# Performance work log

Hardware: AMD Instinct MI355X
Metric: run time of the kernel (lower is better)

Reference implementation:

```python
import jax, jax.numpy as jnp
import numpy as np

EPS = 1e-06


def _phi(x):
    # elu_feature_map: elu(x) + 1  (strictly positive features)
    return jax.nn.elu(x) + 1.0


def setup_inputs() -> dict:
    key = jax.random.key(0)
    k1, k2, k3 = jax.random.split(key, 3)
    N, L, H, D = 4, 4096, 12, 64
    q = jax.random.normal(k1, (N, L, H, D), dtype=jnp.float32)
    k = jax.random.normal(k2, (N, L, H, D), dtype=jnp.float32)
    v = jax.random.normal(k3, (N, L, H, D), dtype=jnp.float32)
    return {"q": q, "k": k, "v": v}


def _causal_linear_attention(q, k, v):
    qf = _phi(q)  # [N,L,H,D]
    kf = _phi(k)
    # normalizer: z_l = q_l . (sum_{s<=l} k_s) + eps
    z = jnp.einsum('nlhd,nlhd->nlh', qf, jnp.cumsum(kf, axis=1)) + EPS
    # causal_dot_product: sequential cumulative outer-product scan over L
    q_l = jnp.moveaxis(qf, 1, 0)  # [L,N,H,D]
    k_l = jnp.moveaxis(kf, 1, 0)
    v_l = jnp.moveaxis(v, 1, 0)   # [L,N,H,M]
    N, H, D = qf.shape[0], qf.shape[2], qf.shape[3]
    M = v.shape[3]
    S0 = jnp.zeros((N, H, D, M), dtype=qf.dtype)

    def step(S, qkv):
        ql, kl, vl = qkv
        S = S + jnp.einsum('nhd,nhm->nhdm', kl, vl)  # accumulate k v^T
        o = jnp.einsum('nhd,nhdm->nhm', ql, S)       # q . S
        return S, o

    _, out = jax.lax.scan(step, S0, (q_l, k_l, v_l))  # out: [L,N,H,M]
    out = jnp.moveaxis(out, 0, 1)  # [N,L,H,M]
    return out / z[..., None]


def reference(q, k, v):
    # mask=None path of LinearAttention.forward (causal linear attention)
    return _causal_linear_attention(q, k, v)
```

## Files before the change

### kernel.cpp

```cpp
#include <hip/hip_runtime.h>


#define NBATCH 4
#define LSEQ   4096
#define NHEAD  12
#define DDIM   64
#define LSTRIDE (NHEAD * DDIM)
#define NH     (NBATCH * NHEAD)
#define EPSF   1e-6f
#define CHUNK  64
#define NUMC   (LSEQ / CHUNK)
#define PPART  32
#define CPP    (NUMC / PPART)
#define SB     72

typedef __attribute__((ext_vector_type(8))) short bf16x8;
typedef __attribute__((ext_vector_type(4))) float f32x4;

__device__ __forceinline__ float phi(float x) { return x > 0.f ? x + 1.f : __expf(x); }
__device__ __forceinline__ float4 phi4(float4 x) {
    float4 r = {phi(x.x), phi(x.y), phi(x.z), phi(x.w)};
    return r;
}

__device__ __forceinline__ unsigned short f2bf(float x) {
    union { float f; unsigned u; } v; v.f = x;
    unsigned r = v.u + 0x7fffu + ((v.u >> 16) & 1u);
    return (unsigned short)(r >> 16);
}
__device__ __forceinline__ float bf2f(short s) {
    union { float f; unsigned u; } v; v.u = ((unsigned)(unsigned short)s) << 16;
    return v.f;
}
__device__ __forceinline__ uint2 pack4(float4 a) {
    uint2 r;
    r.x = (unsigned)f2bf(a.x) | ((unsigned)f2bf(a.y) << 16);
    r.y = (unsigned)f2bf(a.z) | ((unsigned)f2bf(a.w) << 16);
    return r;
}
__device__ __forceinline__ bf16x8 packbf8(float4 a, float4 b) {
    union { bf16x8 v; uint2 u[2]; } r;
    r.u[0] = pack4(a);
    r.u[1] = pack4(b);
    return r.v;
}

__device__ __forceinline__ float4 xpose4(float4 x, int lane) {
    const bool b0 = (lane >> 4) & 1, b1 = (lane >> 5) & 1;
    float s0 = b0 ? x.x : x.y;
    float s1 = b0 ? x.z : x.w;
    s0 = __shfl_xor(s0, 16);
    s1 = __shfl_xor(s1, 16);
    float4 y;
    if (b0) { y.x = s0;  y.y = x.y; y.z = s1;  y.w = x.w; }
    else    { y.x = x.x; y.y = s0;  y.z = x.z; y.w = s1;  }
    float t0 = b1 ? y.x : y.z;
    float t1 = b1 ? y.y : y.w;
    t0 = __shfl_xor(t0, 32);
    t1 = __shfl_xor(t1, 32);
    float4 z;
    if (b1) { z.x = t0;  z.y = t1;  z.z = y.z; z.w = y.w; }
    else    { z.x = y.x; z.y = y.y; z.z = t0;  z.w = t1;  }
    return z;
}

__device__ __forceinline__ void swapbit(uint2& A, uint2& B, int m, bool hi) {
    uint2 t;
    t.x = hi ? A.x : B.x;
    t.y = hi ? A.y : B.y;
    t.x = (unsigned)__shfl_xor((int)t.x, m);
    t.y = (unsigned)__shfl_xor((int)t.y, m);
    if (hi) { A.x = t.x; A.y = t.y; } else { B.x = t.x; B.y = t.y; }
}

__global__ __launch_bounds__(256) void k_pass1(const float* __restrict__ qin,
                                               const float* __restrict__ kin,
                                               const float* __restrict__ vin,
                                               float* __restrict__ kvws,
                                               float* __restrict__ ksws,
                                               float* __restrict__ zws,
                                               float* __restrict__ out) {
    __shared__ short sK [64 * SB];
    __shared__ short sKT[64 * SB];
    __shared__ short sVT[64 * SB];
    __shared__ short sST[64 * SB];
    __shared__ float sKs[64];

    const int b = blockIdx.x, seq = b / PPART, p = b % PPART;
    const int n0 = seq / NHEAD, h0 = seq % NHEAD;
    const int t = threadIdx.x;
    const int lane = t & 63, w = t >> 6;
    const int nn = lane & 15, qq = lane >> 4;
    const int c4 = nn << 2;
    const bool b4 = (lane >> 4) & 1, b5 = (lane >> 5) & 1;

    float4 kreg[4], vreg[4];
    auto LOADKV = [&](int cc) {
        const int gb = ((n0 * LSEQ + (p * CPP + cc) * CHUNK) * NHEAD + h0) * DDIM;
#pragma unroll
        for (int rep = 0; rep < 4; ++rep) {
            const int r16 = rep * 16 + 4 * w + qq;
            kreg[rep] = *(const float4*)(kin + gb + r16 * LSTRIDE + c4);
            vreg[rep] = *(const float4*)(vin + gb + r16 * LSTRIDE + c4);
        }
    };
    auto LOADQ = [&](int cc, bf16x8& o0, bf16x8& o1) {
        const float* qp = qin + ((n0 * LSEQ + (p * CPP + cc) * CHUNK) * NHEAD + h0) * DDIM
                        + (16 * w + nn) * LSTRIDE;
        float4 a = phi4(*(const float4*)(qp + qq * 8));
        float4 bq = phi4(*(const float4*)(qp + qq * 8 + 4));
        float4 cq = phi4(*(const float4*)(qp + 32 + qq * 8));
        float4 dq = phi4(*(const float4*)(qp + 32 + qq * 8 + 4));
        o0 = packbf8(a, bq);
        o1 = packbf8(cq, dq);
    };

    bf16x8 qf0, qf1, qfn0, qfn1;
    LOADKV(0);
    LOADQ(0, qf0, qf1);
    if (t < 64) sKs[t] = 0.f;

    f32x4 Sreg[4] = {{0,0,0,0},{0,0,0,0},{0,0,0,0},{0,0,0,0}};
    float ksTot = 0.f;
    const int iRow = 16 * w + nn;

    for (int cc = 0; cc < CPP; ++cc) {
        const int gbase = ((n0 * LSEQ + (p * CPP + cc) * CHUNK) * NHEAD + h0) * DDIM;
#pragma unroll
        for (int rep = 0; rep < 4; ++rep) {
            const int row = rep * 16 + 4 * w + qq;
            const int l0 = rep * 16 + 4 * w;
            float4 kp = phi4(kreg[rep]);
            *(uint2*)(sK + row * SB + c4) = pack4(kp);
            float4 kt = xpose4(kp, lane);
            *(uint2*)(sKT + (c4 + qq) * SB + l0) = pack4(kt);
            float4 vt = xpose4(vreg[rep], lane);
            *(uint2*)(sVT + (c4 + qq) * SB + l0) = pack4(vt);
        }
        __syncthreads();

        if (cc + 1 < CPP) {
            LOADKV(cc + 1);
            LOADQ(cc + 1, qfn0, qfn1);
        }

        uint2 W[4];
        float zpart = 0.f;
#pragma unroll
        for (int ct = 0; ct < 4; ++ct) {
            bf16x8 kf0 = *(const bf16x8*)(sK + (16 * ct + nn) * SB + qq * 8);
            bf16x8 kf1 = *(const bf16x8*)(sK + (16 * ct + nn) * SB + 32 + qq * 8);
            f32x4 acc = {0.f, 0.f, 0.f, 0.f};
            acc = __builtin_amdgcn_mfma_f32_16x16x32_bf16(kf0, qf0, acc, 0, 0, 0);
            acc = __builtin_amdgcn_mfma_f32_16x16x32_bf16(kf1, qf1, acc, 0, 0, 0);
            float4 mv;
            mv.x = (16 * ct + 4 * qq + 0 <= iRow) ? acc[0] : 0.f;
            mv.y = (16 * ct + 4 * qq + 1 <= iRow) ? acc[1] : 0.f;
            mv.z = (16 * ct + 4 * qq + 2 <= iRow) ? acc[2] : 0.f;
            mv.w = (16 * ct + 4 * qq + 3 <= iRow) ? acc[3] : 0.f;
            zpart += mv.x + mv.y + mv.z + mv.w;
            W[ct] = pack4(mv);
        }
        zpart += __shfl_xor(zpart, 16);
        zpart += __shfl_xor(zpart, 32);
        float zi = zpart;
        if (cc) {
            float zq = 0.f;
#pragma unroll
            for (int j = 0; j < 8; ++j) {
                zq += bf2f(qf0[j]) * sKs[qq * 8 + j];
                zq += bf2f(qf1[j]) * sKs[32 + qq * 8 + j];
            }
            zq += __shfl_xor(zq, 16);
            zq += __shfl_xor(zq, 32);
            zi += zq;
        }

        swapbit(W[0], W[1], 32, b5);
        swapbit(W[2], W[3], 32, b5);
        swapbit(W[0], W[1], 16, b4);
        swapbit(W[2], W[3], 16, b4);
        union U8 { unsigned u[4]; bf16x8 v; };
        U8 a0, a1;
        a0.u[0] = W[0].x; a0.u[1] = W[0].y; a0.u[2] = W[1].x; a0.u[3] = W[1].y;
        a1.u[0] = W[2].x; a1.u[1] = W[2].y; a1.u[2] = W[3].x; a1.u[3] = W[3].y;
        const bf16x8 amB0 = a0.v;
        const bf16x8 amB1 = a1.v;

        f32x4 o[4] = {{0,0,0,0},{0,0,0,0},{0,0,0,0},{0,0,0,0}};
        bf16x8 av0 = *(const bf16x8*)(sVT + iRow * SB + qq * 8);
        bf16x8 av1 = *(const bf16x8*)(sVT + iRow * SB + 32 + qq * 8);
        float ksc = 0.f;
#pragma unroll
        for (int ct = 0; ct < 4; ++ct) {
            bf16x8 vf0 = *(const bf16x8*)(sVT + (16 * ct + nn) * SB + qq * 8);
            bf16x8 vf1 = *(const bf16x8*)(sVT + (16 * ct + nn) * SB + 32 + qq * 8);
            o[ct] = __builtin_amdgcn_mfma_f32_16x16x32_bf16(vf0, amB0, o[ct], 0, 0, 0);
            o[ct] = __builtin_amdgcn_mfma_f32_16x16x32_bf16(vf1, amB1, o[ct], 0, 0, 0);
            if (cc) {
                bf16x8 sf0 = *(const bf16x8*)(sST + (16 * ct + nn) * SB + qq * 8);
                bf16x8 sf1 = *(const bf16x8*)(sST + (16 * ct + nn) * SB + 32 + qq * 8);
                o[ct] = __builtin_amdgcn_mfma_f32_16x16x32_bf16(sf0, qf0, o[ct], 0, 0, 0);
                o[ct] = __builtin_amdgcn_mfma_f32_16x16x32_bf16(sf1, qf1, o[ct], 0, 0, 0);
            }
            bf16x8 kt0 = *(const bf16x8*)(sKT + (16 * ct + nn) * SB + qq * 8);
            bf16x8 kt1 = *(const bf16x8*)(sKT + (16 * ct + nn) * SB + 32 + qq * 8);
            Sreg[ct] = __builtin_amdgcn_mfma_f32_16x16x32_bf16(av0, kt0, Sreg[ct], 0, 0, 0);
            Sreg[ct] = __builtin_amdgcn_mfma_f32_16x16x32_bf16(av1, kt1, Sreg[ct], 0, 0, 0);
            if (ct == w) {
                float s = 0.f;
#pragma unroll
                for (int j = 0; j < 8; ++j) s += bf2f(kt0[j]) + bf2f(kt1[j]);
                s += __shfl_xor(s, 16);
                s += __shfl_xor(s, 32);
                ksc = s;
            }
        }
        ksTot += ksc;

        float* orow = out + gbase + iRow * LSTRIDE;
#pragma unroll
        for (int ct = 0; ct < 4; ++ct)
            *(f32x4*)(orow + 16 * ct + 4 * qq) = o[ct];
        if (qq == 0)
            zws[seq * LSEQ + (p * CPP + cc) * CHUNK + iRow] = zi;

        __syncthreads();
        if (cc + 1 < CPP) {
#pragma unroll
            for (int ct = 0; ct < 4; ++ct)
#pragma unroll
                for (int r = 0; r < 4; ++r)
                    sST[(16 * w + 4 * qq + r) * SB + 16 * ct + nn] = (short)f2bf(Sreg[ct][r]);
            if (qq == 0) sKs[16 * w + nn] += ksc;
            qf0 = qfn0;
            qf1 = qfn1;
        }
    }

    float* kvb = kvws + (size_t)b * (DDIM * DDIM);
#pragma unroll
    for (int ct = 0; ct < 4; ++ct)
#pragma unroll
        for (int r = 0; r < 4; ++r)
            kvb[(16 * w + 4 * qq + r) * DDIM + 16 * ct + nn] = Sreg[ct][r];
    if (qq == 0) ksws[b * DDIM + 16 * w + nn] = ksTot;
}

__global__ __launch_bounds__(64) void k_scanP(float* __restrict__ kv,
                                              float* __restrict__ ksum) {
    const int bid = blockIdx.x;
    const int seq = bid >> 4, part16 = bid & 15;
    const int t = threadIdx.x;
    float4* base = (float4*)(kv + (size_t)seq * PPART * DDIM * DDIM) + part16 * 64 + t;
    float4 S = {0.f, 0.f, 0.f, 0.f};
    for (int b0 = 0; b0 < PPART; b0 += 8) {
        float4 x[8];
#pragma unroll
        for (int j = 0; j < 8; ++j) x[j] = base[(b0 + j) * (DDIM * DDIM / 4)];
#pragma unroll
        for (int j = 0; j < 8; ++j) {
            base[(b0 + j) * (DDIM * DDIM / 4)] = S;
            S.x += x[j].x; S.y += x[j].y; S.z += x[j].z; S.w += x[j].w;
        }
    }
    if (part16 == 0) {
        float* kb = ksum + (size_t)seq * PPART * DDIM + t;
        float s = 0.f;
        for (int b0 = 0; b0 < PPART; b0 += 8) {
            float xs[8];
#pragma unroll
            for (int j = 0; j < 8; ++j) xs[j] = kb[(b0 + j) * DDIM];
#pragma unroll
            for (int j = 0; j < 8; ++j) { kb[(b0 + j) * DDIM] = s; s += xs[j]; }
        }
    }
}

__global__ __launch_bounds__(256) void k_fix(const float* __restrict__ qin,
                                             const float* __restrict__ kvws,
                                             const float* __restrict__ ksws,
                                             const float* __restrict__ zws,
                                             float* __restrict__ out) {
    __shared__ short sST[64 * SB];
    __shared__ float sKs[64];

    const int cg = blockIdx.x;
    const int seq = cg / NUMC, c = cg % NUMC, p = c / CPP;
    const int n0 = seq / NHEAD, h0 = seq % NHEAD;
    const int t = threadIdx.x;
    const int lane = t & 63, w = t >> 6;
    const int nn = lane & 15, qq = lane >> 4;
    const int c4 = nn << 2;
    const int gbase = ((n0 * LSEQ + c * CHUNK) * NHEAD + h0) * DDIM;
    const int iRow = 16 * w + nn;

    if (t < 64) sKs[t] = ksws[(seq * PPART + p) * DDIM + t];

    const float* Sg = kvws + (size_t)(seq * PPART + p) * (DDIM * DDIM);
#pragma unroll
    for (int rep = 0; rep < 4; ++rep) {
        const int row = rep * 16 + 4 * w + qq;
        float4 sv = *(const float4*)(Sg + row * DDIM + c4);
        *(uint2*)(sST + row * SB + c4) = pack4(sv);
    }

    const float* qp = qin + gbase + iRow * LSTRIDE;
    float4 a  = phi4(*(const float4*)(qp + qq * 8));
    float4 bq = phi4(*(const float4*)(qp + qq * 8 + 4));
    float4 cq = phi4(*(const float4*)(qp + 32 + qq * 8));
    float4 dq = phi4(*(const float4*)(qp + 32 + qq * 8 + 4));
    bf16x8 qf0 = packbf8(a, bq);
    bf16x8 qf1 = packbf8(cq, dq);

    float* orow = out + gbase + iRow * LSTRIDE;
    f32x4 o[4];
#pragma unroll
    for (int ct = 0; ct < 4; ++ct)
        o[ct] = *(const f32x4*)(orow + 16 * ct + 4 * qq);
    const float zl = zws[seq * LSEQ + c * CHUNK + iRow];
    __syncthreads();

    float zq = 0.f;
#pragma unroll
    for (int j = 0; j < 8; ++j) {
        zq += bf2f(qf0[j]) * sKs[qq * 8 + j];
        zq += bf2f(qf1[j]) * sKs[32 + qq * 8 + j];
    }
    zq += __shfl_xor(zq, 16);
    zq += __shfl_xor(zq, 32);

#pragma unroll
    for (int ct = 0; ct < 4; ++ct) {
        bf16x8 sf0 = *(const bf16x8*)(sST + (16 * ct + nn) * SB + qq * 8);
        bf16x8 sf1 = *(const bf16x8*)(sST + (16 * ct + nn) * SB + 32 + qq * 8);
        o[ct] = __builtin_amdgcn_mfma_f32_16x16x32_bf16(sf0, qf0, o[ct], 0, 0, 0);
        o[ct] = __builtin_amdgcn_mfma_f32_16x16x32_bf16(sf1, qf1, o[ct], 0, 0, 0);
    }

    const float invz = 1.f / (zl + zq + EPSF);
#pragma unroll
    for (int ct = 0; ct < 4; ++ct) {
        f32x4 r = o[ct];
        r[0] *= invz; r[1] *= invz; r[2] *= invz; r[3] *= invz;
        *(f32x4*)(orow + 16 * ct + 4 * qq) = r;
    }
}

__global__ __launch_bounds__(64) void k_seq(const float* __restrict__ qin,
                                            const float* __restrict__ kin,
                                            const float* __restrict__ vin,
                                            float* __restrict__ out) {
    const int seq = blockIdx.x;
    const int n = seq / NHEAD, h = seq % NHEAD;
    const int lane = threadIdx.x;
    float Scol[DDIM];
#pragma unroll
    for (int d = 0; d < DDIM; ++d) Scol[d] = 0.0f;
    float kc = 0.0f;
    __shared__ float qk[2 * DDIM];
    int base = (n * LSEQ * NHEAD + h) * DDIM + lane;
    for (int i = 0; i < LSEQ; ++i) {
        float qval = phi(qin[base]);
        float kval = phi(kin[base]);
        float vval = vin[base];
        kc += kval;
        float zp = qval * kc;
#pragma unroll
        for (int off = 32; off > 0; off >>= 1) zp += __shfl_xor(zp, off, 64);
        float z = zp + EPSF;
        qk[2 * lane] = kval;
        qk[2 * lane + 1] = qval;
        __syncthreads();
        const float4* qk4 = (const float4*)qk;
        float acc = 0.0f;
#pragma unroll
        for (int d2 = 0; d2 < DDIM / 2; ++d2) {
            float4 t0 = qk4[d2];
            int d = 2 * d2;
            Scol[d]     += t0.x * vval;  acc += t0.y * Scol[d];
            Scol[d + 1] += t0.z * vval;  acc += t0.w * Scol[d + 1];
        }
        out[base] = acc / z;
        base += LSTRIDE;
        __syncthreads();
    }
}

extern "C" void kernel_launch(void* const* d_in, const int* in_sizes, int n_in,
                              void* d_out, int out_size, void* d_ws, size_t ws_size,
                              hipStream_t stream) {
    const float* q = (const float*)d_in[0];
    const float* k = (const float*)d_in[1];
    const float* v = (const float*)d_in[2];
    float* out = (float*)d_out;
    float* ws  = (float*)d_ws;

    const size_t need = ((size_t)NH * PPART * (DDIM * DDIM + DDIM)
                        + (size_t)NH * LSEQ) * sizeof(float);
    if (ws_size >= need) {
        float* kv   = ws;
        float* ksum = kv + (size_t)NH * PPART * DDIM * DDIM;
        float* zws  = ksum + (size_t)NH * PPART * DDIM;
        k_pass1<<<NH * PPART, 256, 0, stream>>>(q, k, v, kv, ksum, zws, out);
        k_scanP<<<NH * 16,     64, 0, stream>>>(kv, ksum);
        k_fix  <<<NH * NUMC,  256, 0, stream>>>(q, kv, ksum, zws, out);
    } else {
        k_seq<<<NH, 64, 0, stream>>>(q, k, v, out);
    }
}
```

Baseline: 224.5 us.

## Make chunk pass fully parallel with one block per chunk

The first pass previously processed two chunks per block sequentially, carrying the running KV state and key sums between chunks. Each block now handles a single 64-row chunk, writes a per-chunk KV state and key sum, and leaves all cross-chunk work to the scan and fix kernels. This doubles the block count and drops the in-block serial dependency. In exchange the KV workspace doubles, the scan kernel now walks 64 chunk states instead of 32, and the fix kernel does the inter-chunk correction for every chunk, including those the first pass used to handle.

```diff
diff --git a/kernel.cpp b/kernel.cpp
--- a/kernel.cpp
+++ b/kernel.cpp
@@ -10,8 +10,6 @@
 #define EPSF   1e-6f
 #define CHUNK  64
 #define NUMC   (LSEQ / CHUNK)
-#define PPART  32
-#define CPP    (NUMC / PPART)
 #define SB     72
 
 typedef __attribute__((ext_vector_type(8))) short bf16x8;
@@ -73,7 +71,7 @@
     if (hi) { A.x = t.x; A.y = t.y; } else { B.x = t.x; B.y = t.y; }
 }
 
-__global__ __launch_bounds__(256) void k_pass1(const float* __restrict__ qin,
+__global__ __launch_bounds__(256) void k_chunk(const float* __restrict__ qin,
                                                const float* __restrict__ kin,
                                                const float* __restrict__ vin,
                                                float* __restrict__ kvws,
@@ -83,160 +81,108 @@
     __shared__ short sK [64 * SB];
     __shared__ short sKT[64 * SB];
     __shared__ short sVT[64 * SB];
-    __shared__ short sST[64 * SB];
-    __shared__ float sKs[64];
-
-    const int b = blockIdx.x, seq = b / PPART, p = b % PPART;
+
+    const int b = blockIdx.x, seq = b / NUMC, c = b % NUMC;
     const int n0 = seq / NHEAD, h0 = seq % NHEAD;
     const int t = threadIdx.x;
     const int lane = t & 63, w = t >> 6;
     const int nn = lane & 15, qq = lane >> 4;
     const int c4 = nn << 2;
     const bool b4 = (lane >> 4) & 1, b5 = (lane >> 5) & 1;
+    const int gbase = ((n0 * LSEQ + c * CHUNK) * NHEAD + h0) * DDIM;
+    const int iRow = 16 * w + nn;
 
     float4 kreg[4], vreg[4];
-    auto LOADKV = [&](int cc) {
-        const int gb = ((n0 * LSEQ + (p * CPP + cc) * CHUNK) * NHEAD + h0) * DDIM;
-#pragma unroll
-        for (int rep = 0; rep < 4; ++rep) {
-            const int r16 = rep * 16 + 4 * w + qq;
-            kreg[rep] = *(const float4*)(kin + gb + r16 * LSTRIDE + c4);
-            vreg[rep] = *(const float4*)(vin + gb + r16 * LSTRIDE + c4);
+#pragma unroll
+    for (int rep = 0; rep < 4; ++rep) {
+        const int r16 = rep * 16 + 4 * w + qq;
+        kreg[rep] = *(const float4*)(kin + gbase + r16 * LSTRIDE + c4);
+        vreg[rep] = *(const float4*)(vin + gbase + r16 * LSTRIDE + c4);
+    }
+    const float* qp = qin + gbase + iRow * LSTRIDE;
+    float4 qa = *(const float4*)(qp + qq * 8);
+    float4 qb = *(const float4*)(qp + qq * 8 + 4);
+    float4 qc = *(const float4*)(qp + 32 + qq * 8);
+    float4 qd = *(const float4*)(qp + 32 + qq * 8 + 4);
+    const bf16x8 qf0 = packbf8(phi4(qa), phi4(qb));
+    const bf16x8 qf1 = packbf8(phi4(qc), phi4(qd));
+
+#pragma unroll
+    for (int rep = 0; rep < 4; ++rep) {
+        const int row = rep * 16 + 4 * w + qq;
+        const int l0 = rep * 16 + 4 * w;
+        float4 kp = phi4(kreg[rep]);
+        *(uint2*)(sK + row * SB + c4) = pack4(kp);
+        float4 kt = xpose4(kp, lane);
+        *(uint2*)(sKT + (c4 + qq) * SB + l0) = pack4(kt);
+        float4 vt = xpose4(vreg[rep], lane);
+        *(uint2*)(sVT + (c4 + qq) * SB + l0) = pack4(vt);
+    }
+    __syncthreads();
+
+    uint2 W[4];
+    float zpart = 0.f;
+#pragma unroll
+    for (int ct = 0; ct < 4; ++ct) {
+        bf16x8 kf0 = *(const bf16x8*)(sK + (16 * ct + nn) * SB + qq * 8);
+        bf16x8 kf1 = *(const bf16x8*)(sK + (16 * ct + nn) * SB + 32 + qq * 8);
+        f32x4 acc = {0.f, 0.f, 0.f, 0.f};
+        acc = __builtin_amdgcn_mfma_f32_16x16x32_bf16(kf0, qf0, acc, 0, 0, 0);
+        acc = __builtin_amdgcn_mfma_f32_16x16x32_bf16(kf1, qf1, acc, 0, 0, 0);
+        float4 mv;
+        mv.x = (16 * ct + 4 * qq + 0 <= iRow) ? acc[0] : 0.f;
+        mv.y = (16 * ct + 4 * qq + 1 <= iRow) ? acc[1] : 0.f;
+        mv.z = (16 * ct + 4 * qq + 2 <= iRow) ? acc[2] : 0.f;
+        mv.w = (16 * ct + 4 * qq + 3 <= iRow) ? acc[3] : 0.f;
+        zpart += mv.x + mv.y + mv.z + mv.w;
+        W[ct] = pack4(mv);
+    }
+    zpart += __shfl_xor(zpart, 16);
+    zpart += __shfl_xor(zpart, 32);
+    const float zi = zpart;
+
+    swapbit(W[0], W[1], 32, b5);
+    swapbit(W[2], W[3], 32, b5);
+    swapbit(W[0], W[1], 16, b4);
+    swapbit(W[2], W[3], 16, b4);
+    union U8 { unsigned u[4]; bf16x8 v; };
+    U8 a0, a1;
+    a0.u[0] = W[0].x; a0.u[1] = W[0].y; a0.u[2] = W[1].x; a0.u[3] = W[1].y;
+    a1.u[0] = W[2].x; a1.u[1] = W[2].y; a1.u[2] = W[3].x; a1.u[3] = W[3].y;
+    const bf16x8 amB0 = a0.v;
+    const bf16x8 amB1 = a1.v;
+
+    f32x4 o[4]    = {{0,0,0,0},{0,0,0,0},{0,0,0,0},{0,0,0,0}};
+    f32x4 Sreg[4] = {{0,0,0,0},{0,0,0,0},{0,0,0,0},{0,0,0,0}};
+    bf16x8 av0 = *(const bf16x8*)(sVT + iRow * SB + qq * 8);
+    bf16x8 av1 = *(const bf16x8*)(sVT + iRow * SB + 32 + qq * 8);
+    float ksc = 0.f;
+#pragma unroll
+    for (int ct = 0; ct < 4; ++ct) {
+        bf16x8 vf0 = *(const bf16x8*)(sVT + (16 * ct + nn) * SB + qq * 8);
+        bf16x8 vf1 = *(const bf16x8*)(sVT + (16 * ct + nn) * SB + 32 + qq * 8);
+        o[ct] = __builtin_amdgcn_mfma_f32_16x16x32_bf16(vf0, amB0, o[ct], 0, 0, 0);
+        o[ct] = __builtin_amdgcn_mfma_f32_16x16x32_bf16(vf1, amB1, o[ct], 0, 0, 0);
+        bf16x8 kt0 = *(const bf16x8*)(sKT + (16 * ct + nn) * SB + qq * 8);
+        bf16x8 kt1 = *(const bf16x8*)(sKT + (16 * ct + nn) * SB + 32 + qq * 8);
+        Sreg[ct] = __builtin_amdgcn_mfma_f32_16x16x32_bf16(av0, kt0, Sreg[ct], 0, 0, 0);
+        Sreg[ct] = __builtin_amdgcn_mfma_f32_16x16x32_bf16(av1, kt1, Sreg[ct], 0, 0, 0);
+        if (ct == w) {
+            float s = 0.f;
+#pragma unroll
+            for (int j = 0; j < 8; ++j) s += bf2f(kt0[j]) + bf2f(kt1[j]);
+            s += __shfl_xor(s, 16);
+            s += __shfl_xor(s, 32);
+            ksc = s;
         }
-    };
-    auto LOADQ = [&](int cc, bf16x8& o0, bf16x8& o1) {
-        const float* qp = qin + ((n0 * LSEQ + (p * CPP + cc) * CHUNK) * NHEAD + h0) * DDIM
-                        + (16 * w + nn) * LSTRIDE;
-        float4 a = phi4(*(const float4*)(qp + qq * 8));
-        float4 bq = phi4(*(const float4*)(qp + qq * 8 + 4));
-        float4 cq = phi4(*(const float4*)(qp + 32 + qq * 8));
-        float4 dq = phi4(*(const float4*)(qp + 32 + qq * 8 + 4));
-        o0 = packbf8(a, bq);
-        o1 = packbf8(cq, dq);
-    };
-
-    bf16x8 qf0, qf1, qfn0, qfn1;
-    LOADKV(0);
-    LOADQ(0, qf0, qf1);
-    if (t < 64) sKs[t] = 0.f;
-
-    f32x4 Sreg[4] = {{0,0,0,0},{0,0,0,0},{0,0,0,0},{0,0,0,0}};
-    float ksTot = 0.f;
-    const int iRow = 16 * w + nn;
-
-    for (int cc = 0; cc < CPP; ++cc) {
-        const int gbase = ((n0 * LSEQ + (p * CPP + cc) * CHUNK) * NHEAD + h0) * DDIM;
-#pragma unroll
-        for (int rep = 0; rep < 4; ++rep) {
-            const int row = rep * 16 + 4 * w + qq;
-            const int l0 = rep * 16 + 4 * w;
-            float4 kp = phi4(kreg[rep]);
-            *(uint2*)(sK + row * SB + c4) = pack4(kp);
-            float4 kt = xpose4(kp, lane);
-            *(uint2*)(sKT + (c4 + qq) * SB + l0) = pack4(kt);
-            float4 vt = xpose4(vreg[rep], lane);
-            *(uint2*)(sVT + (c4 + qq) * SB + l0) = pack4(vt);
-        }
-        __syncthreads();
-
-        if (cc + 1 < CPP) {
-            LOADKV(cc + 1);
-            LOADQ(cc + 1, qfn0, qfn1);
-        }
-
-        uint2 W[4];
-        float zpart = 0.f;
-#pragma unroll
-        for (int ct = 0; ct < 4; ++ct) {
-            bf16x8 kf0 = *(const bf16x8*)(sK + (16 * ct + nn) * SB + qq * 8);
-            bf16x8 kf1 = *(const bf16x8*)(sK + (16 * ct + nn) * SB + 32 + qq * 8);
-            f32x4 acc = {0.f, 0.f, 0.f, 0.f};
-            acc = __builtin_amdgcn_mfma_f32_16x16x32_bf16(kf0, qf0, acc, 0, 0, 0);
-            acc = __builtin_amdgcn_mfma_f32_16x16x32_bf16(kf1, qf1, acc, 0, 0, 0);
-            float4 mv;
-            mv.x = (16 * ct + 4 * qq + 0 <= iRow) ? acc[0] : 0.f;
-            mv.y = (16 * ct + 4 * qq + 1 <= iRow) ? acc[1] : 0.f;
-            mv.z = (16 * ct + 4 * qq + 2 <= iRow) ? acc[2] : 0.f;
-            mv.w = (16 * ct + 4 * qq + 3 <= iRow) ? acc[3] : 0.f;
-            zpart += mv.x + mv.y + mv.z + mv.w;
-            W[ct] = pack4(mv);
-        }
-        zpart += __shfl_xor(zpart, 16);
-        zpart += __shfl_xor(zpart, 32);
-        float zi = zpart;
-        if (cc) {
-            float zq = 0.f;
-#pragma unroll
-            for (int j = 0; j < 8; ++j) {
-                zq += bf2f(qf0[j]) * sKs[qq * 8 + j];
-                zq += bf2f(qf1[j]) * sKs[32 + qq * 8 + j];
-            }
-            zq += __shfl_xor(zq, 16);
-            zq += __shfl_xor(zq, 32);
-            zi += zq;
-        }
-
-        swapbit(W[0], W[1], 32, b5);
-        swapbit(W[2], W[3], 32, b5);
-        swapbit(W[0], W[1], 16, b4);
-        swapbit(W[2], W[3], 16, b4);
-        union U8 { unsigned u[4]; bf16x8 v; };
-        U8 a0, a1;
-        a0.u[0] = W[0].x; a0.u[1] = W[0].y; a0.u[2] = W[1].x; a0.u[3] = W[1].y;
-        a1.u[0] = W[2].x; a1.u[1] = W[2].y; a1.u[2] = W[3].x; a1.u[3] = W[3].y;
-        const bf16x8 amB0 = a0.v;
-        const bf16x8 amB1 = a1.v;
-
-        f32x4 o[4] = {{0,0,0,0},{0,0,0,0},{0,0,0,0},{0,0,0,0}};
-        bf16x8 av0 = *(const bf16x8*)(sVT + iRow * SB + qq * 8);
-        bf16x8 av1 = *(const bf16x8*)(sVT + iRow * SB + 32 + qq * 8);
-        float ksc = 0.f;
-#pragma unroll
-        for (int ct = 0; ct < 4; ++ct) {
-            bf16x8 vf0 = *(const bf16x8*)(sVT + (16 * ct + nn) * SB + qq * 8);
-            bf16x8 vf1 = *(const bf16x8*)(sVT + (16 * ct + nn) * SB + 32 + qq * 8);
-            o[ct] = __builtin_amdgcn_mfma_f32_16x16x32_bf16(vf0, amB0, o[ct], 0, 0, 0);
-            o[ct] = __builtin_amdgcn_mfma_f32_16x16x32_bf16(vf1, amB1, o[ct], 0, 0, 0);
-            if (cc) {
-                bf16x8 sf0 = *(const bf16x8*)(sST + (16 * ct + nn) * SB + qq * 8);
-                bf16x8 sf1 = *(const bf16x8*)(sST + (16 * ct + nn) * SB + 32 + qq * 8);
-                o[ct] = __builtin_amdgcn_mfma_f32_16x16x32_bf16(sf0, qf0, o[ct], 0, 0, 0);
-                o[ct] = __builtin_amdgcn_mfma_f32_16x16x32_bf16(sf1, qf1, o[ct], 0, 0, 0);
-            }
-            bf16x8 kt0 = *(const bf16x8*)(sKT + (16 * ct + nn) * SB + qq * 8);
-            bf16x8 kt1 = *(const bf16x8*)(sKT + (16 * ct + nn) * SB + 32 + qq * 8);
-            Sreg[ct] = __builtin_amdgcn_mfma_f32_16x16x32_bf16(av0, kt0, Sreg[ct], 0, 0, 0);
-            Sreg[ct] = __builtin_amdgcn_mfma_f32_16x16x32_bf16(av1, kt1, Sreg[ct], 0, 0, 0);
-            if (ct == w) {
-                float s = 0.f;
-#pragma unroll
-                for (int j = 0; j < 8; ++j) s += bf2f(kt0[j]) + bf2f(kt1[j]);
-                s += __shfl_xor(s, 16);
-                s += __shfl_xor(s, 32);
-                ksc = s;
-            }
-        }
-        ksTot += ksc;
-
-        float* orow = out + gbase + iRow * LSTRIDE;
-#pragma unroll
-        for (int ct = 0; ct < 4; ++ct)
-            *(f32x4*)(orow + 16 * ct + 4 * qq) = o[ct];
-        if (qq == 0)
-            zws[seq * LSEQ + (p * CPP + cc) * CHUNK + iRow] = zi;
-
-        __syncthreads();
-        if (cc + 1 < CPP) {
-#pragma unroll
-            for (int ct = 0; ct < 4; ++ct)
-#pragma unroll
-                for (int r = 0; r < 4; ++r)
-                    sST[(16 * w + 4 * qq + r) * SB + 16 * ct + nn] = (short)f2bf(Sreg[ct][r]);
-            if (qq == 0) sKs[16 * w + nn] += ksc;
-            qf0 = qfn0;
-            qf1 = qfn1;
-        }
-    }
+    }
+
+    float* orow = out + gbase + iRow * LSTRIDE;
+#pragma unroll
+    for (int ct = 0; ct < 4; ++ct)
+        *(f32x4*)(orow + 16 * ct + 4 * qq) = o[ct];
+    if (qq == 0)
+        zws[seq * LSEQ + c * CHUNK + iRow] = zi;
 
     float* kvb = kvws + (size_t)b * (DDIM * DDIM);
 #pragma unroll
@@ -244,7 +190,7 @@
 #pragma unroll
         for (int r = 0; r < 4; ++r)
             kvb[(16 * w + 4 * qq + r) * DDIM + 16 * ct + nn] = Sreg[ct][r];
-    if (qq == 0) ksws[b * DDIM + 16 * w + nn] = ksTot;
+    if (qq == 0) ksws[b * DDIM + 16 * w + nn] = ksc;
 }
 
 __global__ __launch_bounds__(64) void k_scanP(float* __restrict__ kv,
@@ -252,9 +198,9 @@
     const int bid = blockIdx.x;
     const int seq = bid >> 4, part16 = bid & 15;
     const int t = threadIdx.x;
-    float4* base = (float4*)(kv + (size_t)seq * PPART * DDIM * DDIM) + part16 * 64 + t;
+    float4* base = (float4*)(kv + (size_t)seq * NUMC * DDIM * DDIM) + part16 * 64 + t;
     float4 S = {0.f, 0.f, 0.f, 0.f};
-    for (int b0 = 0; b0 < PPART; b0 += 8) {
+    for (int b0 = 0; b0 < NUMC; b0 += 8) {
         float4 x[8];
 #pragma unroll
         for (int j = 0; j < 8; ++j) x[j] = base[(b0 + j) * (DDIM * DDIM / 4)];
@@ -265,9 +211,9 @@
         }
     }
     if (part16 == 0) {
-        float* kb = ksum + (size_t)seq * PPART * DDIM + t;
+        float* kb = ksum + (size_t)seq * NUMC * DDIM + t;
         float s = 0.f;
-        for (int b0 = 0; b0 < PPART; b0 += 8) {
+        for (int b0 = 0; b0 < NUMC; b0 += 8) {
             float xs[8];
 #pragma unroll
             for (int j = 0; j < 8; ++j) xs[j] = kb[(b0 + j) * DDIM];
@@ -286,7 +232,7 @@
     __shared__ float sKs[64];
 
     const int cg = blockIdx.x;
-    const int seq = cg / NUMC, c = cg % NUMC, p = c / CPP;
+    const int seq = cg / NUMC, c = cg % NUMC;
     const int n0 = seq / NHEAD, h0 = seq % NHEAD;
     const int t = threadIdx.x;
     const int lane = t & 63, w = t >> 6;
@@ -295,9 +241,9 @@
     const int gbase = ((n0 * LSEQ + c * CHUNK) * NHEAD + h0) * DDIM;
     const int iRow = 16 * w + nn;
 
-    if (t < 64) sKs[t] = ksws[(seq * PPART + p) * DDIM + t];
-
-    const float* Sg = kvws + (size_t)(seq * PPART + p) * (DDIM * DDIM);
+    if (t < 64) sKs[t] = ksws[(size_t)cg * DDIM + t];
+
+    const float* Sg = kvws + (size_t)cg * (DDIM * DDIM);
 #pragma unroll
     for (int rep = 0; rep < 4; ++rep) {
         const int row = rep * 16 + 4 * w + qq;
@@ -396,15 +342,15 @@
     float* out = (float*)d_out;
     float* ws  = (float*)d_ws;
 
-    const size_t need = ((size_t)NH * PPART * (DDIM * DDIM + DDIM)
+    const size_t need = ((size_t)NH * NUMC * (DDIM * DDIM + DDIM)
                         + (size_t)NH * LSEQ) * sizeof(float);
     if (ws_size >= need) {
         float* kv   = ws;
-        float* ksum = kv + (size_t)NH * PPART * DDIM * DDIM;
-        float* zws  = ksum + (size_t)NH * PPART * DDIM;
-        k_pass1<<<NH * PPART, 256, 0, stream>>>(q, k, v, kv, ksum, zws, out);
-        k_scanP<<<NH * 16,     64, 0, stream>>>(kv, ksum);
-        k_fix  <<<NH * NUMC,  256, 0, stream>>>(q, kv, ksum, zws, out);
+        float* ksum = kv + (size_t)NH * NUMC * DDIM * DDIM;
+        float* zws  = ksum + (size_t)NH * NUMC * DDIM;
+        k_chunk<<<NH * NUMC, 256, 0, stream>>>(q, k, v, kv, ksum, zws, out);
+        k_scanP<<<NH * 16,    64, 0, stream>>>(kv, ksum);
+        k_fix  <<<NH * NUMC, 256, 0, stream>>>(q, kv, ksum, zws, out);
     } else {
         k_seq<<<NH, 64, 0, stream>>>(q, k, v, out);
     }
```

Measured after the change: 233.8 us. 4.2% more time.
